# Kernel optimization log

Measured on AMD Instinct MI355X. Metric: run time of the kernel, lower is better.

The kernel has to match this reference:

```python
import jax, jax.numpy as jnp
import numpy as np

HEADS = 8
DIM_HEAD = 64
DIM = 512
DIM_INNER = HEADS * DIM_HEAD  # 512
B, N = 4, 1024


def setup_inputs() -> dict:
    key = jax.random.key(0)
    ks = jax.random.split(key, 8)
    s = 0.02
    return {
        "x": jax.random.normal(ks[0], (B, N, DIM), jnp.float32),
        "mask": jnp.ones((B, N), dtype=bool),
        "attn_bias": jax.random.normal(ks[1], (1, HEADS, N, N), jnp.float32),
        "wq": jax.random.normal(ks[2], (DIM_INNER, DIM), jnp.float32) * s,
        "wkv": jax.random.normal(ks[3], (2 * DIM_INNER, DIM), jnp.float32) * s,
        "wo": jax.random.normal(ks[4], (DIM, DIM_INNER), jnp.float32) * s,
        "bo": jax.random.normal(ks[5], (DIM,), jnp.float32) * s,
        "wg": jax.random.normal(ks[6], (DIM_INNER, DIM), jnp.float32) * s,
        "bg": jax.random.normal(ks[7], (DIM_INNER,), jnp.float32) * s,
    }


def reference(x, mask, attn_bias, wq, wkv, wo, bo, wg, bg):
    # Self-attention path: context = x. dropout = 0 (eval).
    scale = DIM_HEAD ** (-0.5)
    b, n, _ = x.shape
    q = (x @ wq.T) * scale                      # [b, n, h*d]
    kv = x @ wkv.T                               # [b, n, 2*h*d]
    k, v = jnp.split(kv, 2, axis=-1)
    q = q.reshape(b, n, HEADS, DIM_HEAD)
    k = k.reshape(b, n, HEADS, DIM_HEAD)
    v = v.reshape(b, n, HEADS, DIM_HEAD)
    dots = jnp.einsum('bihd,bjhd->bhij', q, k) + attn_bias  # [b, h, n, n]
    pair_mask = mask[:, None, :, None] & mask[:, None, None, :]
    mask_value = -jnp.finfo(dots.dtype).max
    dots = jnp.where(pair_mask, dots, mask_value)
    attn = jax.nn.softmax(dots, axis=-1)
    out = jnp.einsum('bhij,bjhd->bihd', attn, v).reshape(b, n, DIM_INNER)
    gates = x @ wg.T + bg                        # gating projection on m = x
    out = out * jax.nn.sigmoid(gates)
    return out @ wo.T + bo
```

## Files before the change

kernel.cpp:

```cpp
#include <hip/hip_runtime.h>
#include <hip/hip_bf16.h>

#define HEADS  8
#define DHEAD  64
#define DIM    512
#define NPROJ  2048
#define BATCH  4
#define SEQ    1024
#define MTOT   (BATCH*SEQ)
#define LOG2E  1.44269504f

typedef __attribute__((ext_vector_type(8))) short          bf16x8;
typedef __attribute__((ext_vector_type(4))) float          f32x4;
typedef __attribute__((ext_vector_type(8))) unsigned short u16x8;
typedef __attribute__((ext_vector_type(4))) unsigned short u16x4;

static __device__ __forceinline__ unsigned short f2bf(float x) {
    unsigned u = __float_as_uint(x);
    u += 0x7fffu + ((u >> 16) & 1u);
    return (unsigned short)(u >> 16);
}
static __device__ __forceinline__ float bf2f(unsigned short b) {
    return __uint_as_float(((unsigned)b) << 16);
}

#define GL_LDS16(gp, lp) __builtin_amdgcn_global_load_lds(                    \
    (__attribute__((address_space(1))) void*)(gp),                            \
    (__attribute__((address_space(3))) void*)(lp), 16, 0, 0)

__global__ __launch_bounds__(256) void cast_kernel(
    const float* __restrict__ x,  const float* __restrict__ wq,
    const float* __restrict__ wkv, const float* __restrict__ wg,
    const float* __restrict__ wo,
    unsigned short* __restrict__ xb, unsigned short* __restrict__ wcat,
    unsigned short* __restrict__ wob)
{
    const int NX = MTOT * DIM / 4;
    const int NW = NPROJ * DIM / 4;
    const int NO = DIM * DIM / 4;
    int i = blockIdx.x * 256 + threadIdx.x;
    if (i < NX) {
        float4 v = ((const float4*)x)[i];
        ushort4 o; o.x = f2bf(v.x); o.y = f2bf(v.y); o.z = f2bf(v.z); o.w = f2bf(v.w);
        ((ushort4*)xb)[i] = o;
    } else if (i < NX + NW) {
        int e   = i - NX;
        int row = e >> 7;
        int c4  = e & 127;
        const float* src; float s = 1.0f;
        if (row < 512)       { src = wq  + row * DIM; s = 0.125f * LOG2E; }
        else if (row < 1536) { src = wkv + (row - 512) * DIM; }
        else                 { src = wg  + (row - 1536) * DIM; }
        float4 v = ((const float4*)src)[c4];
        ushort4 o; o.x = f2bf(v.x*s); o.y = f2bf(v.y*s); o.z = f2bf(v.z*s); o.w = f2bf(v.w*s);
        ((ushort4*)wcat)[e] = o;
    } else if (i < NX + NW + NO) {
        int e = i - NX - NW;
        float4 v = ((const float4*)wo)[e];
        ushort4 o; o.x = f2bf(v.x); o.y = f2bf(v.y); o.z = f2bf(v.z); o.w = f2bf(v.w);
        ((ushort4*)wob)[e] = o;
    }
}

__global__ __launch_bounds__(256) void gemm_qkvg(
    const unsigned short* __restrict__ xb,
    const unsigned short* __restrict__ wcat,
    unsigned short* __restrict__ qkvg)
{
    __shared__ __align__(16) unsigned short As[2][128 * 64];
    __shared__ __align__(16) unsigned short Bs[2][128 * 64];
    const int tid = threadIdx.x;
    const int bm = blockIdx.x, bn = blockIdx.y;
    const int wid = tid >> 6, lane = tid & 63;
    const int wrow = (wid >> 1) * 64, wcol = (wid & 1) * 64;
    const int lr = lane & 15, lg = lane >> 4;

    const int srow = 8 * wid + (lane >> 3);
    const int selem = 8 * (lane & 7);
    const unsigned short* gA = xb   + (size_t)(bm * 128 + srow) * DIM + selem;
    const unsigned short* gB = wcat + (size_t)(bn * 128 + srow) * DIM + selem;

#define QSTAGE(buf, koff)                                                     \
    {                                                                         \
        char* dA = (char*)As[buf] + wid * 1024;                               \
        char* dB = (char*)Bs[buf] + wid * 1024;                               \
        _Pragma("unroll")                                                     \
        for (int j = 0; j < 4; ++j) {                                         \
            GL_LDS16(gA + (size_t)j * 32 * DIM + (koff), dA + j * 4096);      \
            GL_LDS16(gB + (size_t)j * 32 * DIM + (koff), dB + j * 4096);      \
        }                                                                     \
    }

    f32x4 acc[4][4] = {};

    QSTAGE(0, 0);
    __syncthreads();

    for (int kt = 0; kt < 8; ++kt) {
        const int cb = kt & 1;
        if (kt < 7) QSTAGE(cb ^ 1, (kt + 1) * 64);
#pragma unroll
        for (int kk = 0; kk < 2; ++kk) {
            bf16x8 af[4], bfr[4];
#pragma unroll
            for (int mi = 0; mi < 4; ++mi)
                af[mi] = *(const bf16x8*)&As[cb][(wrow + mi * 16 + lr) * 64 + kk * 32 + lg * 8];
#pragma unroll
            for (int ni = 0; ni < 4; ++ni)
                bfr[ni] = *(const bf16x8*)&Bs[cb][(wcol + ni * 16 + lr) * 64 + kk * 32 + lg * 8];
#pragma unroll
            for (int mi = 0; mi < 4; ++mi)
#pragma unroll
                for (int ni = 0; ni < 4; ++ni)
                    acc[mi][ni] = __builtin_amdgcn_mfma_f32_16x16x32_bf16(
                        af[mi], bfr[ni], acc[mi][ni], 0, 0, 0);
        }
        __syncthreads();
    }
#undef QSTAGE

#pragma unroll
    for (int mi = 0; mi < 4; ++mi)
#pragma unroll
        for (int ni = 0; ni < 4; ++ni)
#pragma unroll
            for (int r = 0; r < 4; ++r) {
                int row = bm * 128 + wrow + mi * 16 + lg * 4 + r;
                int col = bn * 128 + wcol + ni * 16 + lr;
                qkvg[(size_t)row * NPROJ + col] = f2bf(acc[mi][ni][r]);
            }
}

#define LDK 72
#define LDV 68
#define NTILES 8
#define DEFER_THR 11.0f

__global__ __launch_bounds__(256, 4) void attn_kernel(
    const unsigned short* __restrict__ qkvg,
    const float* __restrict__ bias,
    float* __restrict__ po,
    float* __restrict__ mbuf,
    float* __restrict__ lbuf)
{
    __shared__ __align__(16) unsigned short Kt[2][64][LDK];
    __shared__ __align__(16) unsigned short Vt[2][64 * LDV];

    const int qb = blockIdx.x * 64;
    const int bh = blockIdx.y;
    const int jh = blockIdx.z;
    const int b = bh >> 3, h = bh & 7;
    const int tid = threadIdx.x, wid = tid >> 6, lane = tid & 63;
    const int lr = lane & 15, lg = lane >> 4;

    const int qrow = qb + wid * 16 + lr;
    const unsigned short* qptr = qkvg + (size_t)(b * SEQ + qrow) * NPROJ + h * DHEAD;
    bf16x8 qf0 = *(const bf16x8*)(qptr + lg * 8);
    bf16x8 qf1 = *(const bf16x8*)(qptr + 32 + lg * 8);

    const float* bptr = bias + ((size_t)h * SEQ + qrow) * SEQ + jh * 512;

    const int srow = tid >> 3, schk = tid & 7;
    const unsigned short* kvb = qkvg +
        (size_t)(b * SEQ + jh * 512 + srow) * NPROJ + h * DHEAD + schk * 8;

    u16x8 kr0 = *(const u16x8*)(kvb + 512);
    u16x8 kr1 = *(const u16x8*)(kvb + 32 * NPROJ + 512);
    u16x8 vr0 = *(const u16x8*)(kvb + 1024);
    u16x8 vr1 = *(const u16x8*)(kvb + 32 * NPROJ + 1024);
    *(u16x8*)&Kt[0][srow][schk * 8]      = kr0;
    *(u16x8*)&Kt[0][srow + 32][schk * 8] = kr1;
#pragma unroll
    for (int e = 0; e < 8; ++e) {
        Vt[0][(schk * 8 + e) * LDV + srow]      = vr0[e];
        Vt[0][(schk * 8 + e) * LDV + srow + 32] = vr1[e];
    }
    f32x4 bv[4], bvn[4];
#pragma unroll
    for (int ji = 0; ji < 4; ++ji) bv[ji] = *(const f32x4*)(bptr + ji * 16 + lg * 4);

    f32x4 oacc[4] = {};
    float mrow = -3.0e38f, lsum = 0.f;

    for (int t = 0; t < NTILES; ++t) {
        const int cur = t & 1;
        __syncthreads();

        if (t < NTILES - 1) {
            const unsigned short* src = kvb + (size_t)(t + 1) * 64 * NPROJ;
            kr0 = *(const u16x8*)(src + 512);
            kr1 = *(const u16x8*)(src + 32 * NPROJ + 512);
            vr0 = *(const u16x8*)(src + 1024);
            vr1 = *(const u16x8*)(src + 32 * NPROJ + 1024);
            const float* bsrc = bptr + (t + 1) * 64;
#pragma unroll
            for (int ji = 0; ji < 4; ++ji)
                bvn[ji] = *(const f32x4*)(bsrc + ji * 16 + lg * 4);
        }

        f32x4 st[4];
        __builtin_amdgcn_s_setprio(1);
#pragma unroll
        for (int ji = 0; ji < 4; ++ji) {
            bf16x8 kf0 = *(const bf16x8*)&Kt[cur][ji * 16 + lr][lg * 8];
            bf16x8 kf1 = *(const bf16x8*)&Kt[cur][ji * 16 + lr][32 + lg * 8];
            f32x4 s = {};
            s = __builtin_amdgcn_mfma_f32_16x16x32_bf16(kf0, qf0, s, 0, 0, 0);
            s = __builtin_amdgcn_mfma_f32_16x16x32_bf16(kf1, qf1, s, 0, 0, 0);
            st[ji] = s;
        }
        __builtin_amdgcn_s_setprio(0);

        float p[4][4];
#pragma unroll
        for (int ji = 0; ji < 4; ++ji)
#pragma unroll
            for (int r = 0; r < 4; ++r)
                p[ji][r] = fmaf(bv[ji][r], LOG2E, st[ji][r]);

        float ta = fmaxf(fmaxf(p[0][0], p[0][1]), fmaxf(p[0][2], p[0][3]));
        float tb = fmaxf(fmaxf(p[1][0], p[1][1]), fmaxf(p[1][2], p[1][3]));
        float tc = fmaxf(fmaxf(p[2][0], p[2][1]), fmaxf(p[2][2], p[2][3]));
        float td = fmaxf(fmaxf(p[3][0], p[3][1]), fmaxf(p[3][2], p[3][3]));
        float tmax = fmaxf(fmaxf(ta, tb), fmaxf(tc, td));
        tmax = fmaxf(tmax, __shfl_xor(tmax, 16));
        tmax = fmaxf(tmax, __shfl_xor(tmax, 32));

        const bool defer = __all(tmax <= mrow + DEFER_THR);
        float rsum = 0.f;
        if (defer) {
#pragma unroll
            for (int ji = 0; ji < 4; ++ji)
#pragma unroll
                for (int r = 0; r < 4; ++r) {
                    float e = __builtin_amdgcn_exp2f(p[ji][r] - mrow);
                    p[ji][r] = e;
                    rsum += e;
                }
            rsum += __shfl_xor(rsum, 16);
            rsum += __shfl_xor(rsum, 32);
            lsum += rsum;
        } else {
            float mnew  = fmaxf(mrow, tmax);
            float alpha = __builtin_amdgcn_exp2f(mrow - mnew);
#pragma unroll
            for (int ji = 0; ji < 4; ++ji)
#pragma unroll
                for (int r = 0; r < 4; ++r) {
                    float e = __builtin_amdgcn_exp2f(p[ji][r] - mnew);
                    p[ji][r] = e;
                    rsum += e;
                }
            rsum += __shfl_xor(rsum, 16);
            rsum += __shfl_xor(rsum, 32);
            lsum = lsum * alpha + rsum;
            mrow = mnew;
#pragma unroll
            for (int di = 0; di < 4; ++di) oacc[di] *= alpha;
        }

        union { unsigned w[4]; bf16x8 v; } pf[2];
#pragma unroll
        for (int c = 0; c < 2; ++c)
#pragma unroll
            for (int w = 0; w < 4; ++w) {
                int ji = 2 * c + (w >> 1), r0 = (w & 1) * 2;
                asm("v_cvt_pk_bf16_f32 %0, %1, %2"
                    : "=v"(pf[c].w[w]) : "v"(p[ji][r0]), "v"(p[ji][r0 + 1]));
            }

        __builtin_amdgcn_s_setprio(1);
#pragma unroll
        for (int di = 0; di < 4; ++di)
#pragma unroll
            for (int c = 0; c < 2; ++c) {
                const unsigned short* vb = &Vt[cur][(di * 16 + lr) * LDV + c * 32 + lg * 4];
                union { u16x4 h[2]; bf16x8 v; } uv;
                uv.h[0] = *(const u16x4*)vb;
                uv.h[1] = *(const u16x4*)(vb + 16);
                oacc[di] = __builtin_amdgcn_mfma_f32_16x16x32_bf16(
                    uv.v, pf[c].v, oacc[di], 0, 0, 0);
            }
        __builtin_amdgcn_s_setprio(0);

        if (t < NTILES - 1) {
            *(u16x8*)&Kt[cur ^ 1][srow][schk * 8]      = kr0;
            *(u16x8*)&Kt[cur ^ 1][srow + 32][schk * 8] = kr1;
#pragma unroll
            for (int e = 0; e < 8; ++e) {
                Vt[cur ^ 1][(schk * 8 + e) * LDV + srow]      = vr0[e];
                Vt[cur ^ 1][(schk * 8 + e) * LDV + srow + 32] = vr1[e];
            }
#pragma unroll
            for (int ji = 0; ji < 4; ++ji) bv[ji] = bvn[ji];
        }
    }

    const size_t row = (size_t)b * SEQ + qrow;
    float* pod = po + (size_t)jh * MTOT * DIM + row * DIM + h * DHEAD;
#pragma unroll
    for (int di = 0; di < 4; ++di)
        *(f32x4*)(pod + di * 16 + lg * 4) = oacc[di];
    if (lg == 0) {
        mbuf[(size_t)jh * MTOT * HEADS + row * HEADS + h] = mrow;
        lbuf[(size_t)jh * MTOT * HEADS + row * HEADS + h] = lsum;
    }
}

__global__ __launch_bounds__(256) void combine_kernel(
    const float* __restrict__ po,
    const float* __restrict__ mbuf, const float* __restrict__ lbuf,
    const unsigned short* __restrict__ qkvg,
    const float* __restrict__ bg,
    unsigned short* __restrict__ obuf)
{
    int idx = blockIdx.x * 256 + threadIdx.x;
    int e0  = idx * 4;
    int row = e0 >> 9;
    int col = e0 & 511;
    int h   = col >> 6;

    float m0 = mbuf[row * HEADS + h];
    float m1 = mbuf[MTOT * HEADS + row * HEADS + h];
    float l0 = lbuf[row * HEADS + h];
    float l1 = lbuf[MTOT * HEADS + row * HEADS + h];
    float ms = fmaxf(m0, m1);
    float w0 = __builtin_amdgcn_exp2f(m0 - ms);
    float w1 = __builtin_amdgcn_exp2f(m1 - ms);
    float rl = 1.f / (l0 * w0 + l1 * w1);

    f32x4 o0 = *(const f32x4*)(po + e0);
    f32x4 o1 = *(const f32x4*)(po + (size_t)MTOT * DIM + e0);
    u16x4 g4 = *(const u16x4*)(qkvg + (size_t)row * NPROJ + 1536 + col);
    f32x4 b4 = *(const f32x4*)(bg + col);

    u16x4 res;
#pragma unroll
    for (int r = 0; r < 4; ++r) {
        float o = (o0[r] * w0 + o1[r] * w1) * rl;
        float gate = bf2f(g4[r]) + b4[r];
        float sg = 1.f / (1.f + __expf(-gate));
        res[r] = f2bf(o * sg);
    }
    *(u16x4*)(obuf + (size_t)row * DIM + col) = res;
}

__global__ __launch_bounds__(256) void gemm_out(
    const unsigned short* __restrict__ obuf,
    const unsigned short* __restrict__ wob,
    const float* __restrict__ bo,
    float* __restrict__ out)
{
    __shared__ __align__(16) unsigned short As[2][64 * 64];
    __shared__ __align__(16) unsigned short Bs[2][64 * 64];
    const int tid = threadIdx.x;
    const int bm = blockIdx.x, bn = blockIdx.y;
    const int wid = tid >> 6, lane = tid & 63;
    const int wrow = (wid >> 1) * 32, wcol = (wid & 1) * 32;
    const int lr = lane & 15, lg = lane >> 4;

    const int srow = 8 * wid + (lane >> 3);
    const int selem = 8 * (lane & 7);
    const unsigned short* gA = obuf + (size_t)(bm * 64 + srow) * DIM + selem;
    const unsigned short* gB = wob  + (size_t)(bn * 64 + srow) * DIM + selem;

#define OSTAGE(buf, koff)                                                     \
    {                                                                         \
        char* dA = (char*)As[buf] + wid * 1024;                               \
        char* dB = (char*)Bs[buf] + wid * 1024;                               \
        _Pragma("unroll")                                                     \
        for (int j = 0; j < 2; ++j) {                                         \
            GL_LDS16(gA + (size_t)j * 32 * DIM + (koff), dA + j * 4096);      \
            GL_LDS16(gB + (size_t)j * 32 * DIM + (koff), dB + j * 4096);      \
        }                                                                     \
    }

    f32x4 acc[2][2] = {};

    OSTAGE(0, 0);
    __syncthreads();

    for (int kt = 0; kt < 8; ++kt) {
        const int cb = kt & 1;
        if (kt < 7) OSTAGE(cb ^ 1, (kt + 1) * 64);
#pragma unroll
        for (int kk = 0; kk < 2; ++kk) {
            bf16x8 af[2], bfr[2];
#pragma unroll
            for (int mi = 0; mi < 2; ++mi)
                af[mi] = *(const bf16x8*)&As[cb][(wrow + mi * 16 + lr) * 64 + kk * 32 + lg * 8];
#pragma unroll
            for (int ni = 0; ni < 2; ++ni)
                bfr[ni] = *(const bf16x8*)&Bs[cb][(wcol + ni * 16 + lr) * 64 + kk * 32 + lg * 8];
#pragma unroll
            for (int mi = 0; mi < 2; ++mi)
#pragma unroll
                for (int ni = 0; ni < 2; ++ni)
                    acc[mi][ni] = __builtin_amdgcn_mfma_f32_16x16x32_bf16(
                        af[mi], bfr[ni], acc[mi][ni], 0, 0, 0);
        }
        __syncthreads();
    }
#undef OSTAGE

#pragma unroll
    for (int mi = 0; mi < 2; ++mi)
#pragma unroll
        for (int ni = 0; ni < 2; ++ni)
#pragma unroll
            for (int r = 0; r < 4; ++r) {
                int row = bm * 64 + wrow + mi * 16 + lg * 4 + r;
                int col = bn * 64 + wcol + ni * 16 + lr;
                out[(size_t)row * DIM + col] = acc[mi][ni][r] + bo[col];
            }
}

extern "C" void kernel_launch(void* const* d_in, const int* in_sizes, int n_in,
                              void* d_out, int out_size, void* d_ws, size_t ws_size,
                              hipStream_t stream)
{
    const float* x    = (const float*)d_in[0];
    const float* bias = (const float*)d_in[2];
    const float* wq   = (const float*)d_in[3];
    const float* wkv  = (const float*)d_in[4];
    const float* wo   = (const float*)d_in[5];
    const float* bo   = (const float*)d_in[6];
    const float* wg   = (const float*)d_in[7];
    const float* bg   = (const float*)d_in[8];
    float* out = (float*)d_out;

    char* ws = (char*)d_ws;
    unsigned short* xb   = (unsigned short*)(ws);
    unsigned short* wcat = (unsigned short*)(ws + 4  * 1024 * 1024);
    unsigned short* wob  = (unsigned short*)(ws + 6  * 1024 * 1024);
    unsigned short* qkvg = (unsigned short*)(ws + 8  * 1024 * 1024);
    unsigned short* obuf = (unsigned short*)(ws + 24 * 1024 * 1024);
    float*          mbuf = (float*)(ws + 28 * 1024 * 1024);
    float*          lbuf = (float*)(ws + 29 * 1024 * 1024);
    float*          po   = (float*)(ws + 32 * 1024 * 1024);

    cast_kernel<<<3328, 256, 0, stream>>>(x, wq, wkv, wg, wo, xb, wcat, wob);
    gemm_qkvg<<<dim3(32, 16), 256, 0, stream>>>(xb, wcat, qkvg);
    attn_kernel<<<dim3(16, 32, 2), 256, 0, stream>>>(qkvg, bias, po, mbuf, lbuf);
    combine_kernel<<<2048, 256, 0, stream>>>(po, mbuf, lbuf, qkvg, bg, obuf);
    gemm_out<<<dim3(64, 8), 256, 0, stream>>>(obuf, wob, bo, out);
}
```

Before: 156.1 us.

## Fuse split-KV combine and gating into attention via in-block LDS merge

The two key-halves of attention now run as two 4-wave groups inside one 512-thread block instead of two separate blocks. They merge their partial outputs through shared memory, reusing the K tile buffer, and apply the sigmoid gate before writing bf16 output. This removes the combine kernel launch and the global round trip of fp32 partial outputs plus m/l buffers. In exchange the block is larger with a doubled LDS footprint, and the final bf16 stores are scalar and strided, which may coalesce poorly.

```diff
diff --git a/kernel.cpp b/kernel.cpp
--- a/kernel.cpp
+++ b/kernel.cpp
@@ -136,44 +136,44 @@
 #define NTILES 8
 #define DEFER_THR 11.0f
 
-__global__ __launch_bounds__(256, 4) void attn_kernel(
+__global__ __launch_bounds__(512, 2) void attn_kernel(
     const unsigned short* __restrict__ qkvg,
     const float* __restrict__ bias,
-    float* __restrict__ po,
-    float* __restrict__ mbuf,
-    float* __restrict__ lbuf)
+    const float* __restrict__ bg,
+    unsigned short* __restrict__ obuf)
 {
-    __shared__ __align__(16) unsigned short Kt[2][64][LDK];
-    __shared__ __align__(16) unsigned short Vt[2][64 * LDV];
+    __shared__ __align__(16) unsigned short Kt[2][2][64][LDK];
+    __shared__ __align__(16) unsigned short Vt[2][2][64 * LDV];
 
     const int qb = blockIdx.x * 64;
     const int bh = blockIdx.y;
-    const int jh = blockIdx.z;
     const int b = bh >> 3, h = bh & 7;
     const int tid = threadIdx.x, wid = tid >> 6, lane = tid & 63;
+    const int jgrp = wid >> 2, wid4 = wid & 3;
     const int lr = lane & 15, lg = lane >> 4;
 
-    const int qrow = qb + wid * 16 + lr;
+    const int qrow = qb + wid4 * 16 + lr;
     const unsigned short* qptr = qkvg + (size_t)(b * SEQ + qrow) * NPROJ + h * DHEAD;
     bf16x8 qf0 = *(const bf16x8*)(qptr + lg * 8);
     bf16x8 qf1 = *(const bf16x8*)(qptr + 32 + lg * 8);
 
-    const float* bptr = bias + ((size_t)h * SEQ + qrow) * SEQ + jh * 512;
-
-    const int srow = tid >> 3, schk = tid & 7;
+    const float* bptr = bias + ((size_t)h * SEQ + qrow) * SEQ + jgrp * 512;
+
+    const int gtid = tid & 255;
+    const int srow = gtid >> 3, schk = gtid & 7;
     const unsigned short* kvb = qkvg +
-        (size_t)(b * SEQ + jh * 512 + srow) * NPROJ + h * DHEAD + schk * 8;
+        (size_t)(b * SEQ + jgrp * 512 + srow) * NPROJ + h * DHEAD + schk * 8;
 
     u16x8 kr0 = *(const u16x8*)(kvb + 512);
     u16x8 kr1 = *(const u16x8*)(kvb + 32 * NPROJ + 512);
     u16x8 vr0 = *(const u16x8*)(kvb + 1024);
     u16x8 vr1 = *(const u16x8*)(kvb + 32 * NPROJ + 1024);
-    *(u16x8*)&Kt[0][srow][schk * 8]      = kr0;
-    *(u16x8*)&Kt[0][srow + 32][schk * 8] = kr1;
+    *(u16x8*)&Kt[jgrp][0][srow][schk * 8]      = kr0;
+    *(u16x8*)&Kt[jgrp][0][srow + 32][schk * 8] = kr1;
 #pragma unroll
     for (int e = 0; e < 8; ++e) {
-        Vt[0][(schk * 8 + e) * LDV + srow]      = vr0[e];
-        Vt[0][(schk * 8 + e) * LDV + srow + 32] = vr1[e];
+        Vt[jgrp][0][(schk * 8 + e) * LDV + srow]      = vr0[e];
+        Vt[jgrp][0][(schk * 8 + e) * LDV + srow + 32] = vr1[e];
     }
     f32x4 bv[4], bvn[4];
 #pragma unroll
@@ -202,8 +202,8 @@
         __builtin_amdgcn_s_setprio(1);
 #pragma unroll
         for (int ji = 0; ji < 4; ++ji) {
-            bf16x8 kf0 = *(const bf16x8*)&Kt[cur][ji * 16 + lr][lg * 8];
-            bf16x8 kf1 = *(const bf16x8*)&Kt[cur][ji * 16 + lr][32 + lg * 8];
+            bf16x8 kf0 = *(const bf16x8*)&Kt[jgrp][cur][ji * 16 + lr][lg * 8];
+            bf16x8 kf1 = *(const bf16x8*)&Kt[jgrp][cur][ji * 16 + lr][32 + lg * 8];
             f32x4 s = {};
             s = __builtin_amdgcn_mfma_f32_16x16x32_bf16(kf0, qf0, s, 0, 0, 0);
             s = __builtin_amdgcn_mfma_f32_16x16x32_bf16(kf1, qf1, s, 0, 0, 0);
@@ -274,7 +274,8 @@
         for (int di = 0; di < 4; ++di)
 #pragma unroll
             for (int c = 0; c < 2; ++c) {
-                const unsigned short* vb = &Vt[cur][(di * 16 + lr) * LDV + c * 32 + lg * 4];
+                const unsigned short* vb =
+                    &Vt[jgrp][cur][(di * 16 + lr) * LDV + c * 32 + lg * 4];
                 union { u16x4 h[2]; bf16x8 v; } uv;
                 uv.h[0] = *(const u16x4*)vb;
                 uv.h[1] = *(const u16x4*)(vb + 16);
@@ -284,65 +285,57 @@
         __builtin_amdgcn_s_setprio(0);
 
         if (t < NTILES - 1) {
-            *(u16x8*)&Kt[cur ^ 1][srow][schk * 8]      = kr0;
-            *(u16x8*)&Kt[cur ^ 1][srow + 32][schk * 8] = kr1;
+            *(u16x8*)&Kt[jgrp][cur ^ 1][srow][schk * 8]      = kr0;
+            *(u16x8*)&Kt[jgrp][cur ^ 1][srow + 32][schk * 8] = kr1;
 #pragma unroll
             for (int e = 0; e < 8; ++e) {
-                Vt[cur ^ 1][(schk * 8 + e) * LDV + srow]      = vr0[e];
-                Vt[cur ^ 1][(schk * 8 + e) * LDV + srow + 32] = vr1[e];
+                Vt[jgrp][cur ^ 1][(schk * 8 + e) * LDV + srow]      = vr0[e];
+                Vt[jgrp][cur ^ 1][(schk * 8 + e) * LDV + srow + 32] = vr1[e];
             }
 #pragma unroll
             for (int ji = 0; ji < 4; ++ji) bv[ji] = bvn[ji];
         }
     }
 
-    const size_t row = (size_t)b * SEQ + qrow;
-    float* pod = po + (size_t)jh * MTOT * DIM + row * DIM + h * DHEAD;
-#pragma unroll
-    for (int di = 0; di < 4; ++di)
-        *(f32x4*)(pod + di * 16 + lg * 4) = oacc[di];
-    if (lg == 0) {
-        mbuf[(size_t)jh * MTOT * HEADS + row * HEADS + h] = mrow;
-        lbuf[(size_t)jh * MTOT * HEADS + row * HEADS + h] = lsum;
-    }
-}
-
-__global__ __launch_bounds__(256) void combine_kernel(
-    const float* __restrict__ po,
-    const float* __restrict__ mbuf, const float* __restrict__ lbuf,
-    const unsigned short* __restrict__ qkvg,
-    const float* __restrict__ bg,
-    unsigned short* __restrict__ obuf)
-{
-    int idx = blockIdx.x * 256 + threadIdx.x;
-    int e0  = idx * 4;
-    int row = e0 >> 9;
-    int col = e0 & 511;
-    int h   = col >> 6;
-
-    float m0 = mbuf[row * HEADS + h];
-    float m1 = mbuf[MTOT * HEADS + row * HEADS + h];
-    float l0 = lbuf[row * HEADS + h];
-    float l1 = lbuf[MTOT * HEADS + row * HEADS + h];
-    float ms = fmaxf(m0, m1);
-    float w0 = __builtin_amdgcn_exp2f(m0 - ms);
-    float w1 = __builtin_amdgcn_exp2f(m1 - ms);
-    float rl = 1.f / (l0 * w0 + l1 * w1);
-
-    f32x4 o0 = *(const f32x4*)(po + e0);
-    f32x4 o1 = *(const f32x4*)(po + (size_t)MTOT * DIM + e0);
-    u16x4 g4 = *(const u16x4*)(qkvg + (size_t)row * NPROJ + 1536 + col);
-    f32x4 b4 = *(const f32x4*)(bg + col);
-
-    u16x4 res;
-#pragma unroll
-    for (int r = 0; r < 4; ++r) {
-        float o = (o0[r] * w0 + o1[r] * w1) * rl;
-        float gate = bf2f(g4[r]) + b4[r];
-        float sg = 1.f / (1.f + __expf(-gate));
-        res[r] = f2bf(o * sg);
-    }
-    *(u16x4*)(obuf + (size_t)row * DIM + col) = res;
+    float* O1  = (float*)&Kt[1][0][0][0];
+    float* m1a = O1 + 64 * 68;
+    float* l1a = m1a + 64;
+    const int qloc = wid4 * 16 + lr;
+
+    __syncthreads();
+    if (jgrp == 1) {
+#pragma unroll
+        for (int di = 0; di < 4; ++di)
+#pragma unroll
+            for (int r = 0; r < 4; ++r)
+                O1[(di * 16 + lg * 4 + r) * 68 + qloc] = oacc[di][r];
+        if (lg == 0) { m1a[qloc] = mrow; l1a[qloc] = lsum; }
+    }
+    __syncthreads();
+    if (jgrp == 0) {
+        float m1v = m1a[qloc], l1v = l1a[qloc];
+        float ms = fmaxf(mrow, m1v);
+        float w0 = __builtin_amdgcn_exp2f(mrow - ms);
+        float w1 = __builtin_amdgcn_exp2f(m1v - ms);
+        float rl = 1.f / (lsum * w0 + l1v * w1);
+
+        const unsigned short* gp = qkvg + (size_t)(b * SEQ + qrow) * NPROJ + 1536 + h * DHEAD;
+        const float* bgp = bg + h * DHEAD;
+#pragma unroll
+        for (int di = 0; di < 4; ++di) {
+            u16x4 g4 = *(const u16x4*)(gp + di * 16 + lg * 4);
+            f32x4 b4 = *(const f32x4*)(bgp + di * 16 + lg * 4);
+#pragma unroll
+            for (int r = 0; r < 4; ++r) {
+                float o1 = O1[(di * 16 + lg * 4 + r) * 68 + qloc];
+                float o = (oacc[di][r] * w0 + o1 * w1) * rl;
+                float gate = bf2f(g4[r]) + b4[r];
+                float sg = 1.f / (1.f + __expf(-gate));
+                int d = di * 16 + lg * 4 + r;
+                obuf[(size_t)(b * SEQ + qrow) * DIM + h * DHEAD + d] = f2bf(o * sg);
+            }
+        }
+    }
 }
 
 __global__ __launch_bounds__(256) void gemm_out(
@@ -435,13 +428,9 @@
     unsigned short* wob  = (unsigned short*)(ws + 6  * 1024 * 1024);
     unsigned short* qkvg = (unsigned short*)(ws + 8  * 1024 * 1024);
     unsigned short* obuf = (unsigned short*)(ws + 24 * 1024 * 1024);
-    float*          mbuf = (float*)(ws + 28 * 1024 * 1024);
-    float*          lbuf = (float*)(ws + 29 * 1024 * 1024);
-    float*          po   = (float*)(ws + 32 * 1024 * 1024);
 
     cast_kernel<<<3328, 256, 0, stream>>>(x, wq, wkv, wg, wo, xb, wcat, wob);
     gemm_qkvg<<<dim3(32, 16), 256, 0, stream>>>(xb, wcat, qkvg);
-    attn_kernel<<<dim3(16, 32, 2), 256, 0, stream>>>(qkvg, bias, po, mbuf, lbuf);
-    combine_kernel<<<2048, 256, 0, stream>>>(po, mbuf, lbuf, qkvg, bg, obuf);
+    attn_kernel<<<dim3(16, 32), 512, 0, stream>>>(qkvg, bias, bg, obuf);
     gemm_out<<<dim3(64, 8), 256, 0, stream>>>(obuf, wob, bo, out);
 }
```

Result: faster. 151.3 us (-3.0%).
